# Performance work log

Hardware: AMD Instinct MI355X
Metric: run time of the kernel (lower is better)

Reference implementation:

```python
import jax, jax.numpy as jnp
import numpy as np

B, N, C, H, NC = 8, 4096, 512, 256, 1000
GRID = 64  # N = GRID*GRID unique positions
LN_EPS = 1e-5


def setup_inputs() -> dict:
    key = jax.random.key(0)
    ks = jax.random.split(key, 10)
    # unique integer grid positions, same for every batch element (original order)
    i = jnp.arange(N)
    base = jnp.stack([i % GRID, i // GRID], axis=-1).astype(jnp.float32)  # [N,2]
    pos_org = jnp.broadcast_to(base, (B, N, 2))
    # per-batch random permutation -> shuffled positions (as the backbone would emit)
    perm = jax.vmap(lambda k: jax.random.permutation(k, N))(jax.random.split(ks[0], B))  # [B,N]
    pos_shuffled = jnp.take_along_axis(pos_org, perm[..., None], axis=1)
    s = 0.02
    return {
        "feat": jax.random.normal(ks[1], (B, N, C), jnp.float32),
        "prev_out": jax.random.normal(ks[2], (B, N, C), jnp.float32),
        "pos_org": pos_org,
        "pos_shuffled": pos_shuffled,
        "proj_W": jax.random.normal(ks[3], (C, C), jnp.float32) * s,
        "proj_b": jnp.zeros((C,), jnp.float32),
        "ln_g": jnp.ones((C,), jnp.float32),
        "ln_b": jnp.zeros((C,), jnp.float32),
        "W1": jax.random.normal(ks[4], (H, C), jnp.float32) * s,
        "b1": jnp.zeros((H,), jnp.float32),
        "W2": jax.random.normal(ks[5], (H, H), jnp.float32) * s,
        "b2": jnp.zeros((H,), jnp.float32),
        "W3": jax.random.normal(ks[6], (NC, H), jnp.float32) * s,
        "b3": jnp.zeros((NC,), jnp.float32),
    }


def _layernorm(x, g, b):
    x32 = x.astype(jnp.float32)
    mu = x32.mean(-1, keepdims=True)
    var = ((x32 - mu) ** 2).mean(-1, keepdims=True)
    return (x32 - mu) * jax.lax.rsqrt(var + LN_EPS) * g + b


def reference(feat, prev_out, pos_org, pos_shuffled, proj_W, proj_b,
              ln_g, ln_b, W1, b1, W2, b2, W3, b3):
    # find_pos_org_order: L1 cdist [B,N,N] + argmin over shuffled axis
    dists = jnp.abs(pos_org[:, :, None, :] - pos_shuffled[:, None, :, :]).sum(-1)
    pos_indices = jnp.argmin(dists, axis=2)  # [B,N]
    # batched gather: feat[b_, pos_indices]
    g = jnp.take_along_axis(feat, pos_indices[..., None], axis=1)  # [B,N,C]
    # fused proj -> layernorm (in fp32) -> cast back -> residual add
    proj = jnp.einsum('bnc,dc->bnd', g, proj_W) + proj_b
    out_feat = prev_out + _layernorm(proj, ln_g, ln_b).astype(feat.dtype)
    # mean-pool over tokens, 3-layer MLP head with relu on first two layers
    pooled = out_feat.mean(1)  # [B,C]
    h = jax.nn.relu(pooled @ W1.T + b1)
    h = jax.nn.relu(h @ W2.T + b2)
    return h @ W3.T + b3  # [B, num_classes]
```

## Files before the change

### kernel.cpp

```cpp
#include <hip/hip_runtime.h>
#include <stdint.h>

#define B_ 8
#define N_ 4096
#define C_ 512
#define H_ 256
#define NC_ 1000

typedef float v4f __attribute__((ext_vector_type(4)));
typedef short v8s __attribute__((ext_vector_type(8)));
typedef unsigned short ushort_t;

__device__ __forceinline__ uint32_t f2bf1(float f) {
    uint32_t u = __float_as_uint(f);
    return (u + 0x7FFFu + ((u >> 16) & 1u)) >> 16;
}
__device__ __forceinline__ uint32_t f2bf2(float lo, float hi) {
    return f2bf1(lo) | (f2bf1(hi) << 16);
}

__global__ void prep_kernel(const float* __restrict__ ps, const float* __restrict__ W,
                            int* __restrict__ inv, ushort_t* __restrict__ Wfrag,
                            float* __restrict__ pooled) {
    int blk = blockIdx.x, t = threadIdx.x;
    if (blk == 0) {
        float4 z = {0.f, 0.f, 0.f, 0.f};
#pragma unroll
        for (int i = 0; i < 4; i++) ((float4*)pooled)[t * 4 + i] = z;
    }
    if (blk < 128) {
        int gid = blk * 256 + t;
        float2 p = ((const float2*)ps)[gid];
        int key = (int)(p.x + 0.5f) + 64 * (int)(p.y + 0.5f);
        int b = gid >> 12;
        inv[(b << 12) + key] = gid & 4095;
    } else {
        int i = (blk - 128) * 256 + t;
        int d = i >> 6, kb = (i >> 2) & 15, q = i & 3;
        const float4* src = (const float4*)(W + d * C_ + kb * 32 + q * 8);
        float4 v0 = src[0], v1 = src[1];
        uint4 pk;
        pk.x = f2bf2(v0.x, v0.y); pk.y = f2bf2(v0.z, v0.w);
        pk.z = f2bf2(v1.x, v1.y); pk.w = f2bf2(v1.z, v1.w);
        ((uint4*)Wfrag)[((d >> 4) * 16 + kb) * 64 + q * 16 + (d & 15)] = pk;
    }
}

__global__ __launch_bounds__(512, 4)
void gemm_ln_pool(const float* __restrict__ feat, const float* __restrict__ prev,
                  const int* __restrict__ inv, const ushort_t* __restrict__ Wfrag,
                  const float* __restrict__ pb, const float* __restrict__ lg,
                  const float* __restrict__ lb, float* __restrict__ pooled) {
    __shared__ v8s Abuf[4096];
    __shared__ float RowS[64], RowQ[64], ColS[512];

    const int t = threadIdx.x;
    const int b = blockIdx.x >> 6;
    const int row0 = (blockIdx.x & 63) << 6;
    const int wv = t >> 6, lane = t & 63, c = lane & 15, q = lane >> 4;

    if (t < 64) { RowS[t] = 0.f; RowQ[t] = 0.f; }

    const int arow = t >> 3;
    const int acol8 = t & 7;
    const int grow = inv[(b << 12) + row0 + arow];
    const float* asrc = feat + ((size_t)(b * N_ + grow) * C_);
#pragma unroll 4
    for (int s = 0; s < 8; s++) {
        const int chunk = s * 8 + acol8;
        float4 f0 = ((const float4*)asrc)[chunk * 2];
        float4 f1 = ((const float4*)asrc)[chunk * 2 + 1];
        uint4 pk;
        pk.x = f2bf2(f0.x, f0.y); pk.y = f2bf2(f0.z, f0.w);
        pk.z = f2bf2(f1.x, f1.y); pk.w = f2bf2(f1.z, f1.w);
        ((uint4*)Abuf)[arow * 64 + (chunk ^ (arow & 7))] = pk;
    }

    const ushort_t* fb[4];
#pragma unroll
    for (int nt = 0; nt < 4; nt++)
        fb[nt] = Wfrag + (wv * 4 + nt) * 8192 + lane * 8;

    const float* psrc = prev + ((b * N_ + row0) * C_) + t;
    float prevsum = 0.f;

    v4f acc[4][4];
    const v4f vzero = {0.f, 0.f, 0.f, 0.f};
#pragma unroll
    for (int mt = 0; mt < 4; mt++)
#pragma unroll
        for (int nt = 0; nt < 4; nt++) acc[mt][nt] = vzero;

    __syncthreads();

#pragma unroll 2
    for (int kb = 0; kb < 16; kb++) {
        v8s af[4], bf[4];
#pragma unroll
        for (int nt = 0; nt < 4; nt++)
            bf[nt] = *((const v8s*)(fb[nt] + kb * 512));
#pragma unroll
        for (int mt = 0; mt < 4; mt++)
            af[mt] = Abuf[(mt * 16 + c) * 64 + ((kb * 4 + q) ^ (c & 7))];
#pragma unroll
        for (int rr = 0; rr < 4; rr++) prevsum += psrc[(kb * 4 + rr) * C_];
#pragma unroll
        for (int mt = 0; mt < 4; mt++)
#pragma unroll
            for (int nt = 0; nt < 4; nt++)
                acc[mt][nt] = __builtin_amdgcn_mfma_f32_16x16x32_bf16(
                    af[mt], bf[nt], acc[mt][nt], 0, 0, 0);
    }

    float pb4[4], lg4[4], lb4[4];
#pragma unroll
    for (int nt = 0; nt < 4; nt++) {
        int n = wv * 64 + nt * 16 + c;
        pb4[nt] = pb[n]; lg4[nt] = lg[n]; lb4[nt] = lb[n];
    }
#pragma unroll
    for (int mt = 0; mt < 4; mt++) {
#pragma unroll
        for (int reg = 0; reg < 4; reg++) {
            float s1 = 0.f, s2 = 0.f;
#pragma unroll
            for (int nt = 0; nt < 4; nt++) {
                float v = acc[mt][nt][reg] + pb4[nt];
                acc[mt][nt][reg] = v;
                s1 += v; s2 += v * v;
            }
#pragma unroll
            for (int d = 1; d < 16; d <<= 1) {
                s1 += __shfl_xor(s1, d);
                s2 += __shfl_xor(s2, d);
            }
            if (c == 0) {
                int r = mt * 16 + q * 4 + reg;
                atomicAdd(&RowS[r], s1);
                atomicAdd(&RowQ[r], s2);
            }
        }
    }
    __syncthreads();
    if (t < 64) {
        float mu = RowS[t] * (1.f / C_);
        float var = RowQ[t] * (1.f / C_) - mu * mu;
        RowS[t] = mu;
        RowQ[t] = rsqrtf(var + 1e-5f);
    }
    __syncthreads();
    float col[4] = {0.f, 0.f, 0.f, 0.f};
#pragma unroll
    for (int mt = 0; mt < 4; mt++) {
#pragma unroll
        for (int reg = 0; reg < 4; reg++) {
            int r = mt * 16 + q * 4 + reg;
            float mu = RowS[r], rs = RowQ[r];
#pragma unroll
            for (int nt = 0; nt < 4; nt++)
                col[nt] += (acc[mt][nt][reg] - mu) * rs * lg4[nt] + lb4[nt];
        }
    }
#pragma unroll
    for (int nt = 0; nt < 4; nt++) {
        col[nt] += __shfl_xor(col[nt], 16);
        col[nt] += __shfl_xor(col[nt], 32);
    }
    if (lane < 16) {
#pragma unroll
        for (int nt = 0; nt < 4; nt++) ColS[wv * 64 + nt * 16 + c] = col[nt];
    }
    __syncthreads();
    atomicAdd(&pooled[b * C_ + t], ColS[t] + prevsum);
}

__global__ __launch_bounds__(1024)
void head12(const float* __restrict__ pooled,
            const float* __restrict__ W1, const float* __restrict__ b1,
            const float* __restrict__ W2, const float* __restrict__ b2,
            float* __restrict__ h2out) {
    __shared__ __align__(16) float P[512];
    __shared__ __align__(16) float H1[256];
    const int b = blockIdx.x, t = threadIdx.x, wv = t >> 6, lane = t & 63;

    for (int i = t; i < 512; i += 1024) P[i] = pooled[b * 512 + i] * (1.f / 4096.f);
    __syncthreads();

#pragma unroll 2
    for (int jj = 0; jj < 16; jj++) {
        const int j = jj * 16 + wv;
        const float4* wr = (const float4*)(W1 + j * C_);
        float4 w0 = wr[lane], w1 = wr[lane + 64];
        float4 p0 = ((const float4*)P)[lane], p1 = ((const float4*)P)[lane + 64];
        float s = w0.x * p0.x + w0.y * p0.y + w0.z * p0.z + w0.w * p0.w
                + w1.x * p1.x + w1.y * p1.y + w1.z * p1.z + w1.w * p1.w;
#pragma unroll
        for (int d = 1; d < 64; d <<= 1) s += __shfl_xor(s, d);
        if (lane == 0) H1[j] = fmaxf(s + b1[j], 0.f);
    }
    __syncthreads();

#pragma unroll 2
    for (int jj = 0; jj < 16; jj++) {
        const int j = jj * 16 + wv;
        float4 w0 = ((const float4*)(W2 + j * H_))[lane];
        float4 p0 = ((const float4*)H1)[lane];
        float s = w0.x * p0.x + w0.y * p0.y + w0.z * p0.z + w0.w * p0.w;
#pragma unroll
        for (int d = 1; d < 64; d <<= 1) s += __shfl_xor(s, d);
        if (lane == 0) h2out[b * H_ + j] = fmaxf(s + b2[j], 0.f);
    }
}

__global__ __launch_bounds__(256)
void head3(const float* __restrict__ h2, const float* __restrict__ W3,
           const float* __restrict__ b3, float* __restrict__ out) {
    const int t = threadIdx.x, wv = t >> 6, lane = t & 63;
    const int b = blockIdx.x / 250;
    const int o = (blockIdx.x % 250) * 4 + wv;
    float4 w0 = ((const float4*)(W3 + o * H_))[lane];
    float4 p0 = ((const float4*)(h2 + b * H_))[lane];
    float s = w0.x * p0.x + w0.y * p0.y + w0.z * p0.z + w0.w * p0.w;
#pragma unroll
    for (int d = 1; d < 64; d <<= 1) s += __shfl_xor(s, d);
    if (lane == 0) out[b * NC_ + o] = s + b3[o];
}

extern "C" void kernel_launch(void* const* d_in, const int* in_sizes, int n_in,
                              void* d_out, int out_size, void* d_ws, size_t ws_size,
                              hipStream_t stream) {
    const float* feat  = (const float*)d_in[0];
    const float* prev  = (const float*)d_in[1];
    const float* ps    = (const float*)d_in[3];
    const float* projW = (const float*)d_in[4];
    const float* pb    = (const float*)d_in[5];
    const float* lg    = (const float*)d_in[6];
    const float* lb    = (const float*)d_in[7];
    const float* W1    = (const float*)d_in[8];
    const float* b1    = (const float*)d_in[9];
    const float* W2    = (const float*)d_in[10];
    const float* b2    = (const float*)d_in[11];
    const float* W3    = (const float*)d_in[12];
    const float* b3    = (const float*)d_in[13];
    float* out = (float*)d_out;

    char* ws = (char*)d_ws;
    ushort_t* Wfrag = (ushort_t*)ws;
    int* inv        = (int*)(ws + 524288);
    float* pooled   = (float*)(ws + 655360);
    float* h2       = (float*)(ws + 671744);

    prep_kernel<<<256, 256, 0, stream>>>(ps, projW, inv, Wfrag, pooled);
    gemm_ln_pool<<<512, 512, 0, stream>>>(feat, prev, inv, Wfrag,
                                          pb, lg, lb, pooled);
    head12<<<8, 1024, 0, stream>>>(pooled, W1, b1, W2, b2, h2);
    head3<<<2000, 256, 0, stream>>>(h2, W3, b3, out);
}
```

Measured before the change: 221.7 us.

## Split prev_out reduction into dedicated blocks, fuse MLP head, use hardware bf16 pack

The summation of prev_out rows moves out of the GEMM blocks into separate interleaved blocks (every third block sums 128 rows), so GEMM blocks no longer carry that strided load traffic inside the MFMA loop. The two head kernels merge into one 200-block kernel in which each block recomputes layers 1 and 2 for its batch element and then produces a 40-column slice of layer 3. This removes one launch and the h2 round-trip through memory, at the cost of redundant W1/W2 work per block. The bf16 packing uses the hardware cvt_pk builtin when it is available.

Result: no change. 219.3 us (-1.1%).

```diff
diff --git a/kernel.cpp b/kernel.cpp
--- a/kernel.cpp
+++ b/kernel.cpp
@@ -15,8 +15,13 @@
     uint32_t u = __float_as_uint(f);
     return (u + 0x7FFFu + ((u >> 16) & 1u)) >> 16;
 }
-__device__ __forceinline__ uint32_t f2bf2(float lo, float hi) {
+__device__ __forceinline__ uint32_t pk2(float lo, float hi) {
+#if __has_builtin(__builtin_amdgcn_cvt_pk_bf16_f32)
+    auto r = __builtin_amdgcn_cvt_pk_bf16_f32(lo, hi);
+    return __builtin_bit_cast(uint32_t, r);
+#else
     return f2bf1(lo) | (f2bf1(hi) << 16);
+#endif
 }
 
 __global__ void prep_kernel(const float* __restrict__ ps, const float* __restrict__ W,
@@ -40,8 +45,8 @@
         const float4* src = (const float4*)(W + d * C_ + kb * 32 + q * 8);
         float4 v0 = src[0], v1 = src[1];
         uint4 pk;
-        pk.x = f2bf2(v0.x, v0.y); pk.y = f2bf2(v0.z, v0.w);
-        pk.z = f2bf2(v1.x, v1.y); pk.w = f2bf2(v1.z, v1.w);
+        pk.x = pk2(v0.x, v0.y); pk.y = pk2(v0.z, v0.w);
+        pk.z = pk2(v1.x, v1.y); pk.w = pk2(v1.z, v1.w);
         ((uint4*)Wfrag)[((d >> 4) * 16 + kb) * 64 + q * 16 + (d & 15)] = pk;
     }
 }
@@ -54,9 +59,29 @@
     __shared__ v8s Abuf[4096];
     __shared__ float RowS[64], RowQ[64], ColS[512];
 
+    const int bid = blockIdx.x;
     const int t = threadIdx.x;
-    const int b = blockIdx.x >> 6;
-    const int row0 = (blockIdx.x & 63) << 6;
+
+    if (bid % 3 == 2) {
+        const int p = bid / 3;
+        const int b = p >> 5;
+        const int r0 = (p & 31) << 7;
+        const float* psrc = prev + ((size_t)(b * N_ + r0) * C_) + t;
+        float s0 = 0.f, s1 = 0.f, s2 = 0.f, s3 = 0.f;
+#pragma unroll 4
+        for (int r = 0; r < 128; r += 4) {
+            s0 += psrc[(r + 0) * C_];
+            s1 += psrc[(r + 1) * C_];
+            s2 += psrc[(r + 2) * C_];
+            s3 += psrc[(r + 3) * C_];
+        }
+        atomicAdd(&pooled[b * C_ + t], (s0 + s1) + (s2 + s3));
+        return;
+    }
+
+    const int gix = (bid / 3) * 2 + (bid % 3);
+    const int b = gix >> 6;
+    const int row0 = (gix & 63) << 6;
     const int wv = t >> 6, lane = t & 63, c = lane & 15, q = lane >> 4;
 
     if (t < 64) { RowS[t] = 0.f; RowQ[t] = 0.f; }
@@ -71,8 +96,8 @@
         float4 f0 = ((const float4*)asrc)[chunk * 2];
         float4 f1 = ((const float4*)asrc)[chunk * 2 + 1];
         uint4 pk;
-        pk.x = f2bf2(f0.x, f0.y); pk.y = f2bf2(f0.z, f0.w);
-        pk.z = f2bf2(f1.x, f1.y); pk.w = f2bf2(f1.z, f1.w);
+        pk.x = pk2(f0.x, f0.y); pk.y = pk2(f0.z, f0.w);
+        pk.z = pk2(f1.x, f1.y); pk.w = pk2(f1.z, f1.w);
         ((uint4*)Abuf)[arow * 64 + (chunk ^ (arow & 7))] = pk;
     }
 
@@ -80,9 +105,6 @@
 #pragma unroll
     for (int nt = 0; nt < 4; nt++)
         fb[nt] = Wfrag + (wv * 4 + nt) * 8192 + lane * 8;
-
-    const float* psrc = prev + ((b * N_ + row0) * C_) + t;
-    float prevsum = 0.f;
 
     v4f acc[4][4];
     const v4f vzero = {0.f, 0.f, 0.f, 0.f};
@@ -102,8 +124,6 @@
 #pragma unroll
         for (int mt = 0; mt < 4; mt++)
             af[mt] = Abuf[(mt * 16 + c) * 64 + ((kb * 4 + q) ^ (c & 7))];
-#pragma unroll
-        for (int rr = 0; rr < 4; rr++) prevsum += psrc[(kb * 4 + rr) * C_];
 #pragma unroll
         for (int mt = 0; mt < 4; mt++)
 #pragma unroll
@@ -171,59 +191,62 @@
         for (int nt = 0; nt < 4; nt++) ColS[wv * 64 + nt * 16 + c] = col[nt];
     }
     __syncthreads();
-    atomicAdd(&pooled[b * C_ + t], ColS[t] + prevsum);
-}
-
-__global__ __launch_bounds__(1024)
-void head12(const float* __restrict__ pooled,
-            const float* __restrict__ W1, const float* __restrict__ b1,
-            const float* __restrict__ W2, const float* __restrict__ b2,
-            float* __restrict__ h2out) {
+    atomicAdd(&pooled[b * C_ + t], ColS[t]);
+}
+
+__global__ __launch_bounds__(256)
+void head_kernel(const float* __restrict__ pooled,
+                 const float* __restrict__ W1, const float* __restrict__ b1,
+                 const float* __restrict__ W2, const float* __restrict__ b2,
+                 const float* __restrict__ W3, const float* __restrict__ b3,
+                 float* __restrict__ out) {
     __shared__ __align__(16) float P[512];
     __shared__ __align__(16) float H1[256];
-    const int b = blockIdx.x, t = threadIdx.x, wv = t >> 6, lane = t & 63;
-
-    for (int i = t; i < 512; i += 1024) P[i] = pooled[b * 512 + i] * (1.f / 4096.f);
-    __syncthreads();
-
-#pragma unroll 2
-    for (int jj = 0; jj < 16; jj++) {
-        const int j = jj * 16 + wv;
-        const float4* wr = (const float4*)(W1 + j * C_);
-        float4 w0 = wr[lane], w1 = wr[lane + 64];
-        float4 p0 = ((const float4*)P)[lane], p1 = ((const float4*)P)[lane + 64];
-        float s = w0.x * p0.x + w0.y * p0.y + w0.z * p0.z + w0.w * p0.w
-                + w1.x * p1.x + w1.y * p1.y + w1.z * p1.z + w1.w * p1.w;
+    __shared__ __align__(16) float H2[256];
+    const int t = threadIdx.x, wv = t >> 6, lane = t & 63;
+    const int b = blockIdx.x / 25;
+    const int slice = blockIdx.x % 25;
+
+    P[t] = pooled[b * C_ + t] * (1.f / 4096.f);
+    P[t + 256] = pooled[b * C_ + t + 256] * (1.f / 4096.f);
+    __syncthreads();
+
+    {
+        const float4* wr = (const float4*)(W1 + t * C_);
+        float s = 0.f;
+#pragma unroll 8
+        for (int k = 0; k < 128; k++) {
+            float4 w = wr[k];
+            float4 p = ((const float4*)P)[k];
+            s += w.x * p.x + w.y * p.y + w.z * p.z + w.w * p.w;
+        }
+        H1[t] = fmaxf(s + b1[t], 0.f);
+    }
+    __syncthreads();
+
+    {
+        const float4* wr = (const float4*)(W2 + t * H_);
+        float s = 0.f;
+#pragma unroll 8
+        for (int k = 0; k < 64; k++) {
+            float4 w = wr[k];
+            float4 p = ((const float4*)H1)[k];
+            s += w.x * p.x + w.y * p.y + w.z * p.z + w.w * p.w;
+        }
+        H2[t] = fmaxf(s + b2[t], 0.f);
+    }
+    __syncthreads();
+
+#pragma unroll
+    for (int jj = 0; jj < 10; jj++) {
+        const int o = slice * 40 + jj * 4 + wv;
+        float4 w = ((const float4*)(W3 + o * H_))[lane];
+        float4 p = ((const float4*)H2)[lane];
+        float s = w.x * p.x + w.y * p.y + w.z * p.z + w.w * p.w;
 #pragma unroll
         for (int d = 1; d < 64; d <<= 1) s += __shfl_xor(s, d);
-        if (lane == 0) H1[j] = fmaxf(s + b1[j], 0.f);
-    }
-    __syncthreads();
-
-#pragma unroll 2
-    for (int jj = 0; jj < 16; jj++) {
-        const int j = jj * 16 + wv;
-        float4 w0 = ((const float4*)(W2 + j * H_))[lane];
-        float4 p0 = ((const float4*)H1)[lane];
-        float s = w0.x * p0.x + w0.y * p0.y + w0.z * p0.z + w0.w * p0.w;
-#pragma unroll
-        for (int d = 1; d < 64; d <<= 1) s += __shfl_xor(s, d);
-        if (lane == 0) h2out[b * H_ + j] = fmaxf(s + b2[j], 0.f);
-    }
-}
-
-__global__ __launch_bounds__(256)
-void head3(const float* __restrict__ h2, const float* __restrict__ W3,
-           const float* __restrict__ b3, float* __restrict__ out) {
-    const int t = threadIdx.x, wv = t >> 6, lane = t & 63;
-    const int b = blockIdx.x / 250;
-    const int o = (blockIdx.x % 250) * 4 + wv;
-    float4 w0 = ((const float4*)(W3 + o * H_))[lane];
-    float4 p0 = ((const float4*)(h2 + b * H_))[lane];
-    float s = w0.x * p0.x + w0.y * p0.y + w0.z * p0.z + w0.w * p0.w;
-#pragma unroll
-    for (int d = 1; d < 64; d <<= 1) s += __shfl_xor(s, d);
-    if (lane == 0) out[b * NC_ + o] = s + b3[o];
+        if (lane == 0) out[b * NC_ + o] = s + b3[o];
+    }
 }
 
 extern "C" void kernel_launch(void* const* d_in, const int* in_sizes, int n_in,
@@ -248,11 +271,9 @@
     ushort_t* Wfrag = (ushort_t*)ws;
     int* inv        = (int*)(ws + 524288);
     float* pooled   = (float*)(ws + 655360);
-    float* h2       = (float*)(ws + 671744);
 
     prep_kernel<<<256, 256, 0, stream>>>(ps, projW, inv, Wfrag, pooled);
-    gemm_ln_pool<<<512, 512, 0, stream>>>(feat, prev, inv, Wfrag,
+    gemm_ln_pool<<<768, 512, 0, stream>>>(feat, prev, inv, Wfrag,
                                           pb, lg, lb, pooled);
-    head12<<<8, 1024, 0, stream>>>(pooled, W1, b1, W2, b2, h2);
-    head3<<<2000, 256, 0, stream>>>(h2, W3, b3, out);
-}
+    head_kernel<<<200, 256, 0, stream>>>(pooled, W1, b1, W2, b2, W3, b3, out);
+}
```
